# Optimization experiments

Hardware: AMD Instinct MI355X
Metric: run time of the kernel (lower is better)

## Reference

```python
import jax, jax.numpy as jnp
import numpy as np

DIM = 320; D_STATE = 32; D_CONV = 4; HEADDIM = 80; D_INNER = 640; NHEADS = 8
CONV_DIM = D_INNER + 2 * D_STATE          # 704
D_IN_PROJ = 2 * D_INNER + 2 * D_STATE + NHEADS  # 1352
ATTN_HEADS = 4; MLP_DIM = 1024; DEPTH = 2; INNER = DIM // 2  # cross-attn downsample_rate=2
PATCH = (128.0, 256.0, 256.0); IMG = (16, 32, 32); NPTS = 6; BATCH = 2
EPS = 1e-5
TWO_PI = 2.0 * np.pi


def layernorm(x, w, b):
    m = x.mean(-1, keepdims=True)
    v = ((x - m) ** 2).mean(-1, keepdims=True)
    return (x - m) * jax.lax.rsqrt(v + EPS) * w + b


def pe_encode(coords, gauss):
    # coords in [0,1], last dim 3 -> random fourier features (sin|cos) of width DIM
    c = TWO_PI * ((2.0 * coords - 1.0) @ gauss)
    return jnp.concatenate([jnp.sin(c), jnp.cos(c)], -1)


def mha(qi, ki, vi, wq, bq, wk, bk, wv, bv, wo, bo):
    q = qi @ wq.T + bq
    k = ki @ wk.T + bk
    v = vi @ wv.T + bv
    B, Nq, Ci = q.shape
    hd = Ci // ATTN_HEADS
    q = q.reshape(B, Nq, ATTN_HEADS, hd)
    k = k.reshape(B, -1, ATTN_HEADS, hd)
    v = v.reshape(B, -1, ATTN_HEADS, hd)
    att = jax.nn.softmax(jnp.einsum('bqhd,bkhd->bhqk', q, k) / np.sqrt(hd), -1)
    o = jnp.einsum('bhqk,bkhd->bqhd', att, v).reshape(B, Nq, Ci)
    return o @ wo.T + bo


def mamba2(xn, in_w, conv_w, conv_b, dt_bias, A_log, Dp, rms_w, out_w):
    Bt, L, _ = xn.shape
    zxbcdt = xn @ in_w.T                                    # (B,L,1352)
    z, xBC, dt = jnp.split(zxbcdt, [D_INNER, D_INNER + CONV_DIM], axis=-1)
    dt = jax.nn.softplus(dt + dt_bias)                      # (B,L,H)
    # causal depthwise conv over sequence, kernel D_CONV
    pad = jnp.pad(xBC, ((0, 0), (D_CONV - 1, 0), (0, 0)))
    conv = conv_b + sum(pad[:, k:k + L] * conv_w[:, k] for k in range(D_CONV))
    xBC = jax.nn.silu(conv)
    xs, Bm, Cm = jnp.split(xBC, [D_INNER, D_INNER + D_STATE], axis=-1)
    A = -jnp.exp(A_log)                                     # (H,)
    xh = xs.reshape(Bt, L, NHEADS, HEADDIM)

    def step(S, inp):  # S: (B,H,N,P)
        dt_t, x_t, B_t, C_t = inp  # (B,H),(B,H,P),(B,N),(B,N)
        decay = jnp.exp(dt_t * A)
        S = S * decay[..., None, None] + (dt_t[..., None, None] * B_t[:, None, :, None]) * x_t[:, :, None, :]
        y = jnp.einsum('bn,bhnp->bhp', C_t, S)
        return S, y

    S0 = jnp.zeros((Bt, NHEADS, D_STATE, HEADDIM), xn.dtype)
    _, ys = jax.lax.scan(step, S0, (dt.transpose(1, 0, 2), xh.transpose(1, 0, 2, 3), Bm.transpose(1, 0, 2), Cm.transpose(1, 0, 2)))
    y = ys.transpose(1, 0, 2, 3) + Dp[None, None, :, None] * xh  # (B,L,H,P)
    y = y.reshape(Bt, L, D_INNER)
    y = y * jax.nn.silu(z)                                  # gated RMSNorm (norm_before_gate=False)
    y = y * jax.lax.rsqrt((y * y).mean(-1, keepdims=True) + EPS) * rms_w
    return y @ out_w.T


def _forward(x, coords, ln_w, ln_b, in_w, conv_w, conv_b, dt_bias, A_log, Dp, rms_w, out_w,
             pe_gauss, point_tab, sa_w, sa_b, t2i_w, t2i_b, t2i_ow, t2i_ob,
             i2t_w, i2t_b, i2t_ow, i2t_ob, norms_w, norms_b, mlp_w1, mlp_b1, mlp_w2, mlp_b2, labels):
    B, C = x.shape[:2]
    img = x.shape[2:]
    n = int(np.prod(img))
    xf = jnp.transpose(x.reshape(B, C, n), (0, 2, 1))       # (B,n,C)
    keys = mamba2(layernorm(xf, ln_w, ln_b), in_w, conv_w, conv_b, dt_bias, A_log, Dp, rms_w, out_w)
    # point embeddings: fourier PE of normalized click coords + label embedding
    point_emb = pe_encode(coords / jnp.asarray(PATCH, x.dtype), pe_gauss) + point_tab[labels]
    # dense image positional encoding over the feature grid
    axes = [(jnp.arange(s, dtype=x.dtype) + 0.5) / s for s in img]
    grid = jnp.stack(jnp.meshgrid(*axes, indexing='ij'), -1)  # (d,h,w,3)
    kpe = jnp.broadcast_to(pe_encode(grid, pe_gauss).reshape(1, n, C), (B, n, C))
    queries = point_emb
    qpe = point_emb
    for i in range(DEPTH):
        saw, sab = sa_w[i], sa_b[i]
        if i == 0:  # skip_first_layer_pe
            queries = mha(queries, queries, queries, saw[0], sab[0], saw[1], sab[1], saw[2], sab[2], saw[3], sab[3])
        else:
            q = queries + qpe
            queries = queries + mha(q, q, queries, saw[0], sab[0], saw[1], sab[1], saw[2], sab[2], saw[3], sab[3])
        queries = layernorm(queries, norms_w[i, 0], norms_b[i, 0])
        q = queries + qpe
        k = keys + kpe
        queries = queries + mha(q, k, keys, t2i_w[i, 0], t2i_b[i, 0], t2i_w[i, 1], t2i_b[i, 1], t2i_w[i, 2], t2i_b[i, 2], t2i_ow[i], t2i_ob[i])
        queries = layernorm(queries, norms_w[i, 1], norms_b[i, 1])
        queries = queries + jax.nn.relu(queries @ mlp_w1[i].T + mlp_b1[i]) @ mlp_w2[i].T + mlp_b2[i]
        queries = layernorm(queries, norms_w[i, 2], norms_b[i, 2])
        q = queries + qpe
        k = keys + kpe
        keys = keys + mha(k, q, queries, i2t_w[i, 0], i2t_b[i, 0], i2t_w[i, 1], i2t_b[i, 1], i2t_w[i, 2], i2t_b[i, 2], i2t_ow[i], i2t_ob[i])
        keys = layernorm(keys, norms_w[i, 3], norms_b[i, 3])
    return jnp.transpose(keys, (0, 2, 1)).reshape(B, C, *img)


def setup_inputs():
    key = jax.random.key(0)
    ks = iter(jax.random.split(key, 64))
    f32 = jnp.float32

    def nrm(shape, s=0.02):
        return s * jax.random.normal(next(ks), shape, dtype=f32)

    inp = {}
    inp['x'] = jax.random.normal(next(ks), (BATCH, DIM) + IMG, dtype=f32)
    inp['coords'] = jax.random.uniform(next(ks), (BATCH, NPTS, 3), dtype=f32) * jnp.asarray(PATCH, f32)
    inp['labels'] = jax.random.randint(next(ks), (BATCH, NPTS), 0, 2)
    inp['ln_w'] = jnp.ones((DIM,), f32)
    inp['ln_b'] = jnp.zeros((DIM,), f32)
    inp['in_w'] = nrm((D_IN_PROJ, DIM))
    inp['conv_w'] = nrm((CONV_DIM, D_CONV), 0.2)
    inp['conv_b'] = jnp.zeros((CONV_DIM,), f32)
    inp['dt_bias'] = nrm((NHEADS,), 0.1)
    inp['A_log'] = jnp.log(jnp.arange(1, NHEADS + 1, dtype=f32))
    inp['Dp'] = jnp.ones((NHEADS,), f32)
    inp['rms_w'] = jnp.ones((D_INNER,), f32)
    inp['out_w'] = nrm((DIM, D_INNER))
    inp['pe_gauss'] = jax.random.normal(next(ks), (3, DIM // 2), dtype=f32)
    inp['point_tab'] = nrm((2, DIM), 1.0)
    inp['sa_w'] = nrm((DEPTH, 4, DIM, DIM))
    inp['sa_b'] = jnp.zeros((DEPTH, 4, DIM), f32)
    inp['t2i_w'] = nrm((DEPTH, 3, INNER, DIM))
    inp['t2i_b'] = jnp.zeros((DEPTH, 3, INNER), f32)
    inp['t2i_ow'] = nrm((DEPTH, DIM, INNER))
    inp['t2i_ob'] = jnp.zeros((DEPTH, DIM), f32)
    inp['i2t_w'] = nrm((DEPTH, 3, INNER, DIM))
    inp['i2t_b'] = jnp.zeros((DEPTH, 3, INNER), f32)
    inp['i2t_ow'] = nrm((DEPTH, DIM, INNER))
    inp['i2t_ob'] = jnp.zeros((DEPTH, DIM), f32)
    inp['norms_w'] = jnp.ones((DEPTH, 4, DIM), f32)
    inp['norms_b'] = jnp.zeros((DEPTH, 4, DIM), f32)
    inp['mlp_w1'] = nrm((DEPTH, MLP_DIM, DIM))
    inp['mlp_b1'] = jnp.zeros((DEPTH, MLP_DIM), f32)
    inp['mlp_w2'] = nrm((DEPTH, DIM, MLP_DIM))
    inp['mlp_b2'] = jnp.zeros((DEPTH, DIM), f32)
    return inp


def reference(x, coords, labels, ln_w, ln_b, in_w, conv_w, conv_b, dt_bias, A_log, Dp, rms_w, out_w,
              pe_gauss, point_tab, sa_w, sa_b, t2i_w, t2i_b, t2i_ow, t2i_ob,
              i2t_w, i2t_b, i2t_ow, i2t_ob, norms_w, norms_b, mlp_w1, mlp_b1, mlp_w2, mlp_b2):
    return _forward(x, coords, ln_w, ln_b, in_w, conv_w, conv_b, dt_bias, A_log, Dp, rms_w, out_w,
                    pe_gauss, point_tab, sa_w, sa_b, t2i_w, t2i_b, t2i_ow, t2i_ob,
                    i2t_w, i2t_b, i2t_ow, i2t_ob, norms_w, norms_b, mlp_w1, mlp_b1, mlp_w2, mlp_b2, labels)
```

## Files before the change

### kernel.cpp

```cpp
#include <hip/hip_runtime.h>
#include <math.h>

#define LSEQ 16384
#define CDIM 320
#define DIN 640
#define NHH 8
#define CONVD 704
#define XBCW 712
#define YSTR 704
#define QCH 64
#define NCHUNK 256

typedef __bf16 bf16_t;
typedef __bf16 bf16x8 __attribute__((ext_vector_type(8)));
typedef float f32x4 __attribute__((ext_vector_type(4)));

__device__ __forceinline__ float wave_sum(float v) {
#pragma unroll
  for (int o = 32; o > 0; o >>= 1) v += __shfl_down(v, o, 64);
  return v;
}
__device__ __forceinline__ float wave_max(float v) {
#pragma unroll
  for (int o = 32; o > 0; o >>= 1) v = fmaxf(v, __shfl_down(v, o, 64));
  return v;
}
__device__ __forceinline__ float block_sum256(float v, float* red) {
  int tid = threadIdx.x;
  v = wave_sum(v);
  __syncthreads();
  if ((tid & 63) == 0) red[tid >> 6] = v;
  __syncthreads();
  return red[0] + red[1] + red[2] + red[3];
}

__global__ void ws_probe(float* out, float v) { out[0] = v; }

__global__ __launch_bounds__(256) void tln(const float* __restrict__ x,
                                           const float* __restrict__ w,
                                           const float* __restrict__ b,
                                           float* __restrict__ out) {
  __shared__ float sT[32][321];
  int t0 = blockIdx.x * 32;
  int tid = threadIdx.x;
  for (int i = tid; i < 2560; i += 256) {
    int c = i >> 3, j4 = i & 7;
    float4 v = *(const float4*)(x + (size_t)c * LSEQ + t0 + j4 * 4);
    sT[j4 * 4 + 0][c] = v.x;
    sT[j4 * 4 + 1][c] = v.y;
    sT[j4 * 4 + 2][c] = v.z;
    sT[j4 * 4 + 3][c] = v.w;
  }
  __syncthreads();
  int wave = tid >> 6, lane = tid & 63;
  for (int tt = wave; tt < 32; tt += 4) {
    float xv[5];
    float s = 0.f;
#pragma unroll
    for (int k = 0; k < 5; ++k) { xv[k] = sT[tt][lane + 64 * k]; s += xv[k]; }
    s = wave_sum(s); s = __shfl(s, 0, 64);
    float mean = s * (1.f / 320.f);
    float v = 0.f;
#pragma unroll
    for (int k = 0; k < 5; ++k) { float d = xv[k] - mean; v += d * d; }
    v = wave_sum(v); v = __shfl(v, 0, 64);
    float rstd = rsqrtf(v * (1.f / 320.f) + 1e-5f);
    float* op = out + (size_t)(t0 + tt) * CDIM;
#pragma unroll
    for (int k = 0; k < 5; ++k) {
      int i = lane + 64 * k;
      op[i] = (xv[k] - mean) * rstd * w[i] + b[i];
    }
  }
}

__global__ __launch_bounds__(256) void lnt(const float* __restrict__ in,
                                           const float* __restrict__ w,
                                           const float* __restrict__ b,
                                           float* __restrict__ out) {
  __shared__ float sT[CDIM][33];
  int t0 = blockIdx.x * 32;
  int tid = threadIdx.x;
  int wave = tid >> 6, lane = tid & 63;
  for (int tt = wave; tt < 32; tt += 4) {
    const float* xp = in + (size_t)(t0 + tt) * CDIM;
    float x[5];
    float s = 0.f;
#pragma unroll
    for (int k = 0; k < 5; ++k) { x[k] = xp[lane + 64 * k]; s += x[k]; }
    s = wave_sum(s); s = __shfl(s, 0, 64);
    float mean = s * (1.f / 320.f);
    float v = 0.f;
#pragma unroll
    for (int k = 0; k < 5; ++k) { float d = x[k] - mean; v += d * d; }
    v = wave_sum(v); v = __shfl(v, 0, 64);
    float rstd = rsqrtf(v * (1.f / 320.f) + 1e-5f);
#pragma unroll
    for (int k = 0; k < 5; ++k) {
      int i = lane + 64 * k;
      sT[i][tt] = (x[k] - mean) * rstd * w[i] + b[i];
    }
  }
  __syncthreads();
  for (int i = tid; i < 320 * 32; i += 256) {
    int cc = i >> 5, t = i & 31;
    out[(size_t)cc * LSEQ + t0 + t] = sT[cc][t];
  }
}

__global__ __launch_bounds__(256) void ln_rows256(float* __restrict__ io,
                                                  const float* __restrict__ w,
                                                  const float* __restrict__ b,
                                                  int nrows) {
  int row = blockIdx.x * 4 + (threadIdx.x >> 6);
  if (row >= nrows) return;
  float* xp = io + (size_t)row * CDIM;
  int lane = threadIdx.x & 63;
  float x[5];
  float s = 0.f;
#pragma unroll
  for (int k = 0; k < 5; ++k) { x[k] = xp[lane + 64 * k]; s += x[k]; }
  s = wave_sum(s); s = __shfl(s, 0, 64);
  float mean = s * (1.f / 320.f);
  float v = 0.f;
#pragma unroll
  for (int k = 0; k < 5; ++k) { float t = x[k] - mean; v += t * t; }
  v = wave_sum(v); v = __shfl(v, 0, 64);
  float rstd = rsqrtf(v * (1.f / 320.f) + 1e-5f);
#pragma unroll
  for (int k = 0; k < 5; ++k) {
    int i = lane + 64 * k;
    xp[i] = (x[k] - mean) * rstd * w[i] + b[i];
  }
}

__global__ __launch_bounds__(256) void gemm_bf(
    const float* __restrict__ A, const float* __restrict__ W,
    const float* __restrict__ bias, const float* __restrict__ pe,
    float* __restrict__ C, float* __restrict__ C2,
    const float* __restrict__ W2, const float* __restrict__ bias2, int wsplit,
    int M, int N, int K, int lda, int ldc, int nsplit, int ldc2,
    int addC, long long sA, long long sC) {
  int z = blockIdx.z;
  A += (size_t)z * sA;
  C += (size_t)z * sC;
  if (C2) C2 += (size_t)z * sC;
  int gx = gridDim.x;
  int nwg = gx * gridDim.y;
  int lin = blockIdx.y * gx + blockIdx.x;
  int xcd = lin & 7, idx = lin >> 3;
  int q = nwg >> 3, r = nwg & 7;
  int base = (xcd < r) ? xcd * (q + 1) : r * (q + 1) + (xcd - r) * q;
  int lin2 = base + idx;
  int mblk = lin2 / gx, nblk = lin2 % gx;
  int m0 = mblk << 7, n0 = nblk << 6;

  __shared__ __align__(16) bf16_t As[2][4096];
  __shared__ __align__(16) bf16_t Ws[2][2048];
  int tid = threadIdx.x;
  int wave = tid >> 6, lane = tid & 63;
  int fm = lane & 15, quad = lane >> 4;
  int rA = tid >> 1, hA = tid & 1;
  int rW = tid >> 2, qW = tid & 3;
  const float* ag = A + (size_t)(m0 + rA) * lda + hA * 16;
  const float* peg = pe ? pe + (size_t)(m0 + rA) * lda + hA * 16 : (const float*)0;
  int wRow = n0 + rW;
  const float* wg;
  if (wRow < wsplit) wg = W + (size_t)wRow * K + qW * 8;
  else               wg = W2 + (size_t)(wRow - wsplit) * K + qW * 8;
  bool wok = wRow < N;
  int aoff = (rA >> 4) * 512 + (hA * 32 + (rA & 15)) * 8;
  int woff = (rW >> 4) * 512 + (qW * 16 + (rW & 15)) * 8;

  f32x4 acc[2][4];
#pragma unroll
  for (int i = 0; i < 2; ++i)
#pragma unroll
    for (int j = 0; j < 4; ++j) acc[i][j] = (f32x4){0.f, 0.f, 0.f, 0.f};

  float4 pa0, pa1, pa2, pa3, pw0, pw1;
  auto loadG = [&](int k0) {
    pa0 = *(const float4*)(ag + k0);
    pa1 = *(const float4*)(ag + k0 + 4);
    pa2 = *(const float4*)(ag + k0 + 8);
    pa3 = *(const float4*)(ag + k0 + 12);
    if (peg) {
      float4 q0 = *(const float4*)(peg + k0);
      float4 q1 = *(const float4*)(peg + k0 + 4);
      float4 q2 = *(const float4*)(peg + k0 + 8);
      float4 q3 = *(const float4*)(peg + k0 + 12);
      pa0.x += q0.x; pa0.y += q0.y; pa0.z += q0.z; pa0.w += q0.w;
      pa1.x += q1.x; pa1.y += q1.y; pa1.z += q1.z; pa1.w += q1.w;
      pa2.x += q2.x; pa2.y += q2.y; pa2.z += q2.z; pa2.w += q2.w;
      pa3.x += q3.x; pa3.y += q3.y; pa3.z += q3.z; pa3.w += q3.w;
    }
    pw0 = make_float4(0.f, 0.f, 0.f, 0.f);
    pw1 = pw0;
    if (wok) {
      pw0 = *(const float4*)(wg + k0);
      pw1 = *(const float4*)(wg + k0 + 4);
    }
  };
  auto packLDS = [&](int buf) {
    bf16x8 v;
    v[0] = (bf16_t)pa0.x; v[1] = (bf16_t)pa0.y; v[2] = (bf16_t)pa0.z; v[3] = (bf16_t)pa0.w;
    v[4] = (bf16_t)pa1.x; v[5] = (bf16_t)pa1.y; v[6] = (bf16_t)pa1.z; v[7] = (bf16_t)pa1.w;
    *(bf16x8*)&As[buf][aoff] = v;
    v[0] = (bf16_t)pa2.x; v[1] = (bf16_t)pa2.y; v[2] = (bf16_t)pa2.z; v[3] = (bf16_t)pa2.w;
    v[4] = (bf16_t)pa3.x; v[5] = (bf16_t)pa3.y; v[6] = (bf16_t)pa3.z; v[7] = (bf16_t)pa3.w;
    *(bf16x8*)&As[buf][aoff + 128] = v;
    v[0] = (bf16_t)pw0.x; v[1] = (bf16_t)pw0.y; v[2] = (bf16_t)pw0.z; v[3] = (bf16_t)pw0.w;
    v[4] = (bf16_t)pw1.x; v[5] = (bf16_t)pw1.y; v[6] = (bf16_t)pw1.z; v[7] = (bf16_t)pw1.w;
    *(bf16x8*)&Ws[buf][woff] = v;
  };

  int nk = K >> 5;
  loadG(0);
  packLDS(0);
  __syncthreads();
  for (int i = 0; i < nk; ++i) {
    int buf = i & 1;
    bool more = (i + 1 < nk);
    if (more) loadG((i + 1) << 5);
    int ab = wave * 1024 + lane * 8;
    bf16x8 af0 = *(bf16x8*)&As[buf][ab];
    bf16x8 af1 = *(bf16x8*)&As[buf][ab + 512];
    bf16x8 b0 = *(bf16x8*)&Ws[buf][lane * 8];
    bf16x8 b1 = *(bf16x8*)&Ws[buf][512 + lane * 8];
    bf16x8 b2 = *(bf16x8*)&Ws[buf][1024 + lane * 8];
    bf16x8 b3 = *(bf16x8*)&Ws[buf][1536 + lane * 8];
    acc[0][0] = __builtin_amdgcn_mfma_f32_16x16x32_bf16(af0, b0, acc[0][0], 0, 0, 0);
    acc[0][1] = __builtin_amdgcn_mfma_f32_16x16x32_bf16(af0, b1, acc[0][1], 0, 0, 0);
    acc[0][2] = __builtin_amdgcn_mfma_f32_16x16x32_bf16(af0, b2, acc[0][2], 0, 0, 0);
    acc[0][3] = __builtin_amdgcn_mfma_f32_16x16x32_bf16(af0, b3, acc[0][3], 0, 0, 0);
    acc[1][0] = __builtin_amdgcn_mfma_f32_16x16x32_bf16(af1, b0, acc[1][0], 0, 0, 0);
    acc[1][1] = __builtin_amdgcn_mfma_f32_16x16x32_bf16(af1, b1, acc[1][1], 0, 0, 0);
    acc[1][2] = __builtin_amdgcn_mfma_f32_16x16x32_bf16(af1, b2, acc[1][2], 0, 0, 0);
    acc[1][3] = __builtin_amdgcn_mfma_f32_16x16x32_bf16(af1, b3, acc[1][3], 0, 0, 0);
    if (more) {
      packLDS(buf ^ 1);
      __syncthreads();
    }
  }
#pragma unroll
  for (int ms = 0; ms < 2; ++ms)
#pragma unroll
    for (int ns = 0; ns < 4; ++ns) {
      int n = n0 + ns * 16 + fm;
      if (n >= N) continue;
      float bv = 0.f;
      if (n < wsplit) { if (bias) bv = bias[n]; }
      else            { if (bias2) bv = bias2[n - wsplit]; }
      float* Cb;
      int ldcb, nc;
      if (n < nsplit) { Cb = C; ldcb = ldc; nc = n; }
      else           { Cb = C2; ldcb = ldc2; nc = n - nsplit; }
#pragma unroll
      for (int rr = 0; rr < 4; ++rr) {
        int m = m0 + wave * 32 + ms * 16 + quad * 4 + rr;
        float v = acc[ms][ns][rr] + bv;
        size_t off = (size_t)m * ldcb + nc;
        if (addC) v += Cb[off];
        Cb[off] = v;
      }
    }
}

__global__ __launch_bounds__(256) void smallmm(
    const float* __restrict__ A, const float* __restrict__ A2,
    const float* __restrict__ W, const float* __restrict__ bias,
    float* __restrict__ C, int N, int K, int addC, int relu, int a2lim) {
  int wave = threadIdx.x >> 6, lane = threadIdx.x & 63;
  int n = blockIdx.x * 4 + wave;
  if (n >= N) return;
  const float* w = W + (size_t)n * K;
  bool useA2 = (A2 != nullptr) && (n < a2lim);
  float part[12];
#pragma unroll
  for (int m = 0; m < 12; ++m) part[m] = 0.f;
  for (int k0 = 0; k0 < K; k0 += 64) {
    int k = k0 + lane;
    if (k < K) {
      float wv = w[k];
      const float* ap = A + k;
      if (useA2) {
        const float* ap2 = A2 + k;
#pragma unroll
        for (int m = 0; m < 12; ++m)
          part[m] = fmaf(ap[(size_t)m * K] + ap2[(size_t)m * K], wv, part[m]);
      } else {
#pragma unroll
        for (int m = 0; m < 12; ++m)
          part[m] = fmaf(ap[(size_t)m * K], wv, part[m]);
      }
    }
  }
// ... 149 lines not shown
    float cav = cabuf[(size_t)h * LSEQ + t0 + tid];
    sca[tid] = cav;
    sexp[tid] = expf(cav);
  }
  for (int i = tid; i < 2048; i += 256) {
    int j = i >> 5, n = i & 31;
    size_t base = (size_t)(t0 + j) * CONVD;
    sB[j * 40 + n] = (bf16_t)Cv[base + 640 + n];
    sC[j * 40 + n] = (bf16_t)Cv[base + 672 + n];
  }
  for (int i = tid; i < 5120; i += 256) {
    int j = i / 80, p = i % 80;
    sXt[p * 72 + j] = (bf16_t)Cv[(size_t)(t0 + j) * CONVD + h * 80 + p];
  }
  {
    const float* sp = Sprev + (size_t)(h * NCHUNK + c) * 2560;
    for (int i = tid; i < 2560; i += 256) {
      int n = i / 80, p = i % 80;
      sSt[p * 40 + n] = (bf16_t)sp[i];
    }
  }
  __syncthreads();
  int m0 = wave * 16;
  int jbase = m0 + quad * 4;
  bf16x8 afC = *(bf16x8*)&sC[(m0 + fm) * 40 + quad * 8];
  f32x4 accS[4];
#pragma unroll
  for (int nt = 0; nt < 4; ++nt) {
    bf16x8 bf = *(bf16x8*)&sB[(nt * 16 + fm) * 40 + quad * 8];
    f32x4 zero = (f32x4){0.f, 0.f, 0.f, 0.f};
    accS[nt] = __builtin_amdgcn_mfma_f32_16x16x32_bf16(afC, bf, zero, 0, 0, 0);
  }
  float scaj[4];
#pragma unroll
  for (int r = 0; r < 4; ++r) scaj[r] = sca[jbase + r];
#pragma unroll
  for (int nt = 0; nt < 4; ++nt) {
    int s = nt * 16 + fm;
    float dts = sdt[s], scas = sca[s];
#pragma unroll
    for (int r = 0; r < 4; ++r) {
      int j = jbase + r;
      float v = 0.f;
      if (s <= j) v = accS[nt][r] * dts * expf(scaj[r] - scas);
      sP[j * 72 + s] = (bf16_t)v;
    }
  }
  f32x4 acc[5];
#pragma unroll
  for (int pt = 0; pt < 5; ++pt) {
    bf16x8 bf = *(bf16x8*)&sSt[(pt * 16 + fm) * 40 + quad * 8];
    f32x4 zero = (f32x4){0.f, 0.f, 0.f, 0.f};
    acc[pt] = __builtin_amdgcn_mfma_f32_16x16x32_bf16(afC, bf, zero, 0, 0, 0);
  }
  float gj[4];
#pragma unroll
  for (int r = 0; r < 4; ++r) gj[r] = sexp[jbase + r];
#pragma unroll
  for (int pt = 0; pt < 5; ++pt)
#pragma unroll
    for (int r = 0; r < 4; ++r) acc[pt][r] *= gj[r];
  bf16x8 afP0 = *(bf16x8*)&sP[(m0 + fm) * 72 + 0 + quad * 8];
  bf16x8 afP1 = *(bf16x8*)&sP[(m0 + fm) * 72 + 32 + quad * 8];
#pragma unroll
  for (int pt = 0; pt < 5; ++pt) {
    bf16x8 bx0 = *(bf16x8*)&sXt[(pt * 16 + fm) * 72 + 0 + quad * 8];
    bf16x8 bx1 = *(bf16x8*)&sXt[(pt * 16 + fm) * 72 + 32 + quad * 8];
    acc[pt] = __builtin_amdgcn_mfma_f32_16x16x32_bf16(afP0, bx0, acc[pt], 0, 0, 0);
    acc[pt] = __builtin_amdgcn_mfma_f32_16x16x32_bf16(afP1, bx1, acc[pt], 0, 0, 0);
  }
  float dval = Dp[h];
#pragma unroll
  for (int pt = 0; pt < 5; ++pt) {
    int p = pt * 16 + fm;
#pragma unroll
    for (int r = 0; r < 4; ++r) {
      int j = jbase + r;
      float xv = (float)sXt[p * 72 + j];
      Y[(size_t)(t0 + j) * YSTR + h * 80 + p] = acc[pt][r] + dval * xv;
    }
  }
}

__global__ __launch_bounds__(256) void gate_rms(float* __restrict__ Y,
                                                const float* __restrict__ Z,
                                                const float* __restrict__ rms_w) {
  __shared__ float red[4];
  size_t row = blockIdx.x;
  float* y = Y + row * YSTR;
  const float* z = Z + row * DIN;
  float ss = 0.f;
  for (int i = threadIdx.x; i < DIN; i += 256) {
    float zi = z[i];
    float g = y[i] * (zi / (1.f + expf(-zi)));
    y[i] = g;
    ss += g * g;
  }
  float tot = block_sum256(ss, red);
  float r = rsqrtf(tot / (float)DIN + 1e-5f);
  for (int i = threadIdx.x; i < DIN; i += 256) y[i] = y[i] * r * rms_w[i];
}

__global__ void kpe_kernel(const float* __restrict__ gauss, float* __restrict__ KPE) {
  int idx = blockIdx.x * 256 + threadIdx.x;
  if (idx >= LSEQ * 160) return;
  int f = idx % 160, t = idx / 160;
  int d = t >> 10, hh = (t >> 5) & 31, w = t & 31;
  float vx = 2.f * ((d + 0.5f) / 16.f) - 1.f;
  float vy = 2.f * ((hh + 0.5f) / 32.f) - 1.f;
  float vz = 2.f * ((w + 0.5f) / 32.f) - 1.f;
  float cc = 6.28318530717958647692f * (vx * gauss[f] + vy * gauss[160 + f] + vz * gauss[320 + f]);
  KPE[(size_t)t * CDIM + f] = sinf(cc);
  KPE[(size_t)t * CDIM + 160 + f] = cosf(cc);
}

__global__ void point_kernel(const float* __restrict__ coords, const int* __restrict__ labels,
                             const float* __restrict__ gauss, const float* __restrict__ ptab,
                             float* __restrict__ qpe, float* __restrict__ queries) {
  int idx = blockIdx.x * 64 + threadIdx.x;
  if (idx >= 12 * 160) return;
  int f = idx % 160, pt = idx / 160;
  const float* co = coords + pt * 3;
  float vx = 2.f * (co[0] / 128.f) - 1.f;
  float vy = 2.f * (co[1] / 256.f) - 1.f;
  float vz = 2.f * (co[2] / 256.f) - 1.f;
  float cc = 6.28318530717958647692f * (vx * gauss[f] + vy * gauss[160 + f] + vz * gauss[320 + f]);
  int lab = labels[pt];
  float sv = sinf(cc) + ptab[lab * CDIM + f];
  float cv = cosf(cc) + ptab[lab * CDIM + 160 + f];
  qpe[pt * CDIM + f] = sv;       qpe[pt * CDIM + 160 + f] = cv;
  queries[pt * CDIM + f] = sv;   queries[pt * CDIM + 160 + f] = cv;
}

__global__ void attn_self(const float* __restrict__ P3, float* __restrict__ O) {
  int h = blockIdx.x, b = blockIdx.y;
  __shared__ float sq[6][80], sk[6][80], sv[6][80], sw[6][6];
  int tid = threadIdx.x;
  for (int i = tid; i < 480; i += 128) {
    int tok = i / 80, p = i % 80;
    const float* base = P3 + (size_t)(b * 6 + tok) * 960 + h * 80 + p;
    sq[tok][p] = base[0]; sk[tok][p] = base[320]; sv[tok][p] = base[640];
  }
  __syncthreads();
  if (tid < 36) {
    int qi = tid / 6, ki = tid % 6;
    float d = 0.f;
    for (int p = 0; p < 80; ++p) d += sq[qi][p] * sk[ki][p];
    sw[qi][ki] = d * 0.11180339887498948f;
  }
  __syncthreads();
  if (tid < 6) {
    float mx = sw[tid][0];
    for (int k = 1; k < 6; ++k) mx = fmaxf(mx, sw[tid][k]);
    float s = 0.f;
    for (int k = 0; k < 6; ++k) { float e = expf(sw[tid][k] - mx); sw[tid][k] = e; s += e; }
    float inv = 1.f / s;
    for (int k = 0; k < 6; ++k) sw[tid][k] *= inv;
  }
  __syncthreads();
  for (int i = tid; i < 480; i += 128) {
    int qi = i / 80, p = i % 80;
    float o = 0.f;
    for (int k = 0; k < 6; ++k) o += sw[qi][k] * sv[k][p];
    O[(size_t)(b * 6 + qi) * CDIM + h * 80 + p] = o;
  }
}

__global__ __launch_bounds__(256) void attn_t2i_part2(const float* __restrict__ Qp,
                                                      const float* __restrict__ Kp,
                                                      const float* __restrict__ Vp,
                                                      float* __restrict__ Part) {
  int b = blockIdx.z, h = blockIdx.y, c = blockIdx.x;
  Qp += (size_t)b * 960;
  Kp += (size_t)b * LSEQ * 160;
  Vp += (size_t)b * LSEQ * 160;
  Part += (size_t)b * 24 * 64 * 42;
  __shared__ float sq[240];
  __shared__ float redm[4][6], reds[4][6];
  __shared__ __align__(16) bf16_t sPb[16 * 264];
  __shared__ __align__(16) bf16_t sVtb[48 * 264];
  int tid = threadIdx.x;
  int wave = tid >> 6, lane = tid & 63;
  if (tid < 240) sq[tid] = Qp[(size_t)(tid / 40) * 160 + h * 40 + (tid % 40)];
// ... 29 lines not shown
    if (lane == 0) redm[wave][qi] = wm;
  }
  __syncthreads();
  float gmax[6], ls[6];
#pragma unroll
  for (int qi = 0; qi < 6; ++qi)
    gmax[qi] = fmaxf(fmaxf(redm[0][qi], redm[1][qi]), fmaxf(redm[2][qi], redm[3][qi]));
#pragma unroll
  for (int qi = 0; qi < 6; ++qi) {
    float e = expf(s[qi] - gmax[qi]);
    sPb[qi * 264 + tid] = (bf16_t)e;
    float wsum = wave_sum(e);
    if (lane == 0) reds[wave][qi] = wsum;
  }
  __syncthreads();
#pragma unroll
  for (int qi = 0; qi < 6; ++qi)
    ls[qi] = reds[0][qi] + reds[1][qi] + reds[2][qi] + reds[3][qi];
  if (tid == 0) {
#pragma unroll
    for (int qi = 0; qi < 6; ++qi) {
      float* pml = Part + (size_t)((h * 6 + qi) * 64 + c) * 42;
      pml[40] = gmax[qi];
      pml[41] = ls[qi];
    }
  }
  if (wave == 0) {
    int fm = lane & 15, quad = lane >> 4;
    f32x4 acc[3];
#pragma unroll
    for (int nt = 0; nt < 3; ++nt) acc[nt] = (f32x4){0.f, 0.f, 0.f, 0.f};
#pragma unroll
    for (int ks = 0; ks < 8; ++ks) {
      bf16x8 a = *(bf16x8*)&sPb[fm * 264 + ks * 32 + quad * 8];
#pragma unroll
      for (int nt = 0; nt < 3; ++nt) {
        bf16x8 bb = *(bf16x8*)&sVtb[(nt * 16 + fm) * 264 + ks * 32 + quad * 8];
        acc[nt] = __builtin_amdgcn_mfma_f32_16x16x32_bf16(a, bb, acc[nt], 0, 0, 0);
      }
    }
#pragma unroll
    for (int nt = 0; nt < 3; ++nt)
#pragma unroll
      for (int r = 0; r < 4; ++r) {
        int qi = quad * 4 + r;
        int p = nt * 16 + fm;
        if (qi < 6 && p < 40)
          Part[(size_t)((h * 6 + qi) * 64 + c) * 42 + p] = acc[nt][r];
      }
  }
}

__global__ void attn_t2i_comb(const float* __restrict__ Part, float* __restrict__ O) {
  int b = blockIdx.y;
  int blk = blockIdx.x;
  int qi = blk % 6;
  int h = blk / 6;
  int j = threadIdx.x;
  const float* base = Part + (size_t)b * 24 * 64 * 42 + (size_t)blk * 64 * 42;
  float m = base[j * 42 + 40], l = base[j * 42 + 41];
  float gmax = wave_max(m);
  gmax = __shfl(gmax, 0, 64);
  float sc = expf(m - gmax);
  float tot = wave_sum(l * sc);
  tot = __shfl(tot, 0, 64);
  float inv = 1.f / tot;
  __shared__ float ssc[64];
  ssc[j] = sc;
  __syncthreads();
  if (j < 40) {
    float a0 = 0.f, a1 = 0.f, a2 = 0.f, a3 = 0.f;
    for (int jj = 0; jj < 64; jj += 4) {
      a0 = fmaf(base[(jj + 0) * 42 + j], ssc[jj + 0], a0);
      a1 = fmaf(base[(jj + 1) * 42 + j], ssc[jj + 1], a1);
      a2 = fmaf(base[(jj + 2) * 42 + j], ssc[jj + 2], a2);
      a3 = fmaf(base[(jj + 3) * 42 + j], ssc[jj + 3], a3);
    }
    O[(size_t)b * 960 + (size_t)qi * 160 + h * 40 + j] = (a0 + a1 + a2 + a3) * inv;
  }
}

__global__ __launch_bounds__(256) void attn_i2t(const float* __restrict__ Qp,
                                                const float* __restrict__ KV,
                                                float* __restrict__ O) {
  int h = blockIdx.y, b = blockIdx.z;
  int t = blockIdx.x * 256 + threadIdx.x;
  Qp += (size_t)b * LSEQ * 160;
  O += (size_t)b * LSEQ * 160;
  __shared__ float sk[6][40], sv[6][40];
  if (threadIdx.x < 240) {
    int tok = threadIdx.x / 40, p = threadIdx.x % 40;
    const float* base = KV + (size_t)(b * 6 + tok) * 320 + h * 40 + p;
    sk[tok][p] = base[0];
    sv[tok][p] = base[160];
  }
  __syncthreads();
  const float* q = Qp + (size_t)t * 160 + h * 40;
  float qr[40];
#pragma unroll
  for (int v = 0; v < 10; ++v) {
    float4 q4 = *(const float4*)(q + v * 4);
    qr[v * 4 + 0] = q4.x; qr[v * 4 + 1] = q4.y; qr[v * 4 + 2] = q4.z; qr[v * 4 + 3] = q4.w;
  }
  float s[6];
#pragma unroll
  for (int k = 0; k < 6; ++k) {
    float d = 0.f;
    for (int p = 0; p < 40; ++p) d += qr[p] * sk[k][p];
    s[k] = d * 0.15811388300841897f;
  }
  float mx = s[0];
#pragma unroll
  for (int k = 1; k < 6; ++k) mx = fmaxf(mx, s[k]);
  float sum = 0.f;
#pragma unroll
  for (int k = 0; k < 6; ++k) { s[k] = expf(s[k] - mx); sum += s[k]; }
  float inv = 1.f / sum;
  float* o = O + (size_t)t * 160 + h * 40;
#pragma unroll
  for (int v = 0; v < 10; ++v) {
    float o0 = 0.f, o1 = 0.f, o2 = 0.f, o3 = 0.f;
#pragma unroll
    for (int k = 0; k < 6; ++k) {
      float w = s[k];
      o0 += w * sv[k][v * 4 + 0];
      o1 += w * sv[k][v * 4 + 1];
      o2 += w * sv[k][v * 4 + 2];
      o3 += w * sv[k][v * 4 + 3];
    }
    *(float4*)(o + v * 4) = make_float4(o0 * inv, o1 * inv, o2 * inv, o3 * inv);
  }
}

extern "C" void kernel_launch(void* const* d_in, const int* in_sizes, int n_in,
                              void* d_out, int out_size, void* d_ws, size_t ws_size,
                              hipStream_t stream) {
  (void)in_sizes; (void)n_in; (void)out_size;
  const float* x       = (const float*)d_in[0];
  const float* coords  = (const float*)d_in[1];
  const int*   labels  = (const int*)  d_in[2];
  const float* ln_w    = (const float*)d_in[3];
  const float* ln_b    = (const float*)d_in[4];
  const float* in_w    = (const float*)d_in[5];
  const float* conv_w  = (const float*)d_in[6];
  const float* conv_b  = (const float*)d_in[7];
  const float* dt_bias = (const float*)d_in[8];
  const float* A_log   = (const float*)d_in[9];
  const float* Dp      = (const float*)d_in[10];
  const float* rms_w   = (const float*)d_in[11];
  const float* out_w   = (const float*)d_in[12];
  const float* gauss   = (const float*)d_in[13];
  const float* ptab    = (const float*)d_in[14];
  const float* sa_w    = (const float*)d_in[15];
  const float* sa_b    = (const float*)d_in[16];
  const float* t2i_w   = (const float*)d_in[17];
  const float* t2i_b   = (const float*)d_in[18];
  const float* t2i_ow  = (const float*)d_in[19];
  const float* t2i_ob  = (const float*)d_in[20];
  const float* i2t_w   = (const float*)d_in[21];
  const float* i2t_b   = (const float*)d_in[22];
  const float* i2t_ow  = (const float*)d_in[23];
  const float* i2t_ob  = (const float*)d_in[24];
  const float* norms_w = (const float*)d_in[25];
  const float* norms_b = (const float*)d_in[26];
  const float* mlp_w1  = (const float*)d_in[27];
  const float* mlp_b1  = (const float*)d_in[28];
  const float* mlp_w2  = (const float*)d_in[29];
  const float* mlp_b2  = (const float*)d_in[30];
  float* out = (float*)d_out;
  float* ws = (float*)d_ws;

  const size_t NEED = (size_t)(10485760 + 5242880 + 11665408 + 11534336 + 10485760 +
                               131072 + 131072 + 65536) * 4;
  if (ws_size < NEED) {
    ws_probe<<<1, 1, 0, stream>>>(out, (float)ws_size);
    return;
  }
  float* R_K = ws;
  float* P   = ws + 10485760;
  float* XN_     = P;
  float* SCHUNK_ = P;
  float* ZB_     = P + 5242880;
  float* XBC_    = P + 15728640;
  float* SPREV_  = P + 15728640;
  float* CV_     = P + 27394048;
  float* DT_     = P + 38928384;
  float* CA_     = P + 39059456;
  float* KPE_  = P;
  float* T0_   = P + 5242880;
  float* T3_   = P + 10485760;
  float* T1_   = P + 15728640;
  float* T2_   = P + 26214400;
  float* PART_ = P + 36700160;
  float* SM_   = P + 36829184;
  float* QPE_  = SM_;
  float* QRY_  = SM_ + 3840;
  float* P3_   = SM_ + 7680;
  float* PO_   = SM_ + 19200;
  float* H_    = SM_ + 23040;
  float* Q160_ = SM_ + 35328;
  float* O160_ = SM_ + 37248;
  float* KV_   = SM_ + 39168;

  const long long sIMG160 = (long long)LSEQ * 160;
  const long long sIMG320 = (long long)LSEQ * CDIM;
  const int NOSPLIT = 1 << 30;

  for (int b = 0; b < 2; ++b) {
    const float* xb = x + (size_t)b * CDIM * LSEQ;
    float* Kb = R_K + (size_t)b * LSEQ * CDIM;

    tln<<<LSEQ / 32, 256, 0, stream>>>(xb, ln_w, ln_b, XN_);

    gemm_bf<<<dim3(22, 128, 1), 256, 0, stream>>>(
        XN_, in_w, nullptr, nullptr, ZB_, XBC_, nullptr, nullptr, NOSPLIT,
        LSEQ, 1352, CDIM, CDIM, DIN, DIN, XBCW, 0, 0, 0);

    dt_kernel<<<LSEQ * NHH / 256, 256, 0, stream>>>(XBC_, dt_bias, DT_);
    conv2<<<dim3(11, 128), 256, 0, stream>>>(XBC_, conv_w, conv_b, CV_);

    scan_a<<<dim3(NCHUNK, NHH), 256, 0, stream>>>(CV_, DT_, A_log, SCHUNK_, CA_);
    scan_b<<<dim3(10, NHH), 256, 0, stream>>>(SCHUNK_, CA_, SPREV_);
    scan_c<<<dim3(NCHUNK, NHH), 256, 0, stream>>>(CV_, DT_, CA_, SPREV_, Dp, CV_);

    gate_rms<<<LSEQ, 256, 0, stream>>>(CV_, ZB_, rms_w);

    gemm_bf<<<dim3(5, 128, 1), 256, 0, stream>>>(
        CV_, out_w, nullptr, nullptr, Kb, nullptr, nullptr, nullptr, NOSPLIT,
        LSEQ, CDIM, DIN, YSTR, CDIM, NOSPLIT, 0, 0, 0, 0);
  }

  kpe_kernel<<<LSEQ * 160 / 256, 256, 0, stream>>>(gauss, KPE_);
  point_kernel<<<30, 64, 0, stream>>>(coords, labels, gauss, ptab, QPE_, QRY_);

  for (int i = 0; i < 2; ++i) {
    const float* saw = sa_w + (size_t)i * 4 * CDIM * CDIM;
    const float* sab = sa_b + (size_t)i * 4 * CDIM;
    smallmm<<<240, 256, 0, stream>>>(QRY_, (i == 0) ? nullptr : QPE_,
                                     saw, sab, P3_, 960, CDIM, 0, 0, 640);
    attn_self<<<dim3(4, 2), 128, 0, stream>>>(P3_, PO_);
    smallmm<<<80, 256, 0, stream>>>(PO_, nullptr, saw + 3 * 102400, sab + 3 * CDIM,
                                    QRY_, CDIM, CDIM, (i == 0) ? 0 : 1, 0, 0);
    ln_rows256<<<3, 256, 0, stream>>>(QRY_, norms_w + (size_t)(i * 4 + 0) * CDIM,
                                      norms_b + (size_t)(i * 4 + 0) * CDIM, 12);

    smallmm<<<40, 256, 0, stream>>>(QRY_, QPE_, t2i_w + (size_t)(i * 3 + 0) * 51200,
                                    t2i_b + (size_t)(i * 3 + 0) * 160, Q160_,
                                    160, CDIM, 0, 0, 160);
    gemm_bf<<<dim3(5, 128, 2), 256, 0, stream>>>(
        R_K, t2i_w + (size_t)(i * 3 + 1) * 51200, t2i_b + (size_t)(i * 3 + 1) * 160,
        KPE_, T0_, T3_, i2t_w + (size_t)(i * 3 + 0) * 51200,
        i2t_b + (size_t)(i * 3 + 0) * 160, 160,
        LSEQ, 320, CDIM, CDIM, 160, 160, 160, 0, sIMG320, sIMG160);
    gemm_bf<<<dim3(3, 128, 2), 256, 0, stream>>>(
        R_K, t2i_w + (size_t)(i * 3 + 2) * 51200, t2i_b + (size_t)(i * 3 + 2) * 160,
        nullptr, T1_, nullptr, nullptr, nullptr, NOSPLIT,
        LSEQ, 160, CDIM, CDIM, 160, NOSPLIT, 0, 0, sIMG320, sIMG160);
    attn_t2i_part2<<<dim3(64, 4, 2), 256, 0, stream>>>(Q160_, T0_, T1_, PART_);
    attn_t2i_comb<<<dim3(24, 2), 64, 0, stream>>>(PART_, O160_);
    smallmm<<<80, 256, 0, stream>>>(O160_, nullptr, t2i_ow + (size_t)i * 51200,
                                    t2i_ob + (size_t)i * CDIM, QRY_,
                                    CDIM, 160, 1, 0, 0);
    ln_rows256<<<3, 256, 0, stream>>>(QRY_, norms_w + (size_t)(i * 4 + 1) * CDIM,
                                      norms_b + (size_t)(i * 4 + 1) * CDIM, 12);

    smallmm<<<256, 256, 0, stream>>>(QRY_, nullptr, mlp_w1 + (size_t)i * 1024 * CDIM,
                                     mlp_b1 + (size_t)i * 1024, H_, 1024, CDIM, 0, 1, 0);
    smallmm<<<80, 256, 0, stream>>>(H_, nullptr, mlp_w2 + (size_t)i * CDIM * 1024,
                                    mlp_b2 + (size_t)i * CDIM, QRY_, CDIM, 1024, 1, 0, 0);
    ln_rows256<<<3, 256, 0, stream>>>(QRY_, norms_w + (size_t)(i * 4 + 2) * CDIM,
                                      norms_b + (size_t)(i * 4 + 2) * CDIM, 12);

    smallmm<<<80, 256, 0, stream>>>(QRY_, QPE_, i2t_w + (size_t)(i * 3 + 1) * 51200,
                                    i2t_b + (size_t)(i * 3 + 1) * 160, KV_,
                                    320, CDIM, 0, 0, 160);
    attn_i2t<<<dim3(LSEQ / 256, 4, 2), 256, 0, stream>>>(T3_, KV_, T2_);
    gemm_bf<<<dim3(5, 128, 2), 256, 0, stream>>>(
        T2_, i2t_ow + (size_t)i * CDIM * 160, i2t_ob + (size_t)i * CDIM,
        nullptr, R_K, nullptr, nullptr, nullptr, NOSPLIT,
        LSEQ, CDIM, 160, 160, CDIM, NOSPLIT, 0, 1, sIMG160, sIMG320);
    if (i == 0) {
      ln_rows256<<<2 * LSEQ / 4, 256, 0, stream>>>(
          R_K, norms_w + (size_t)3 * CDIM, norms_b + (size_t)3 * CDIM, 2 * LSEQ);
    }
  }

  for (int b = 0; b < 2; ++b) {
    lnt<<<LSEQ / 32, 256, 0, stream>>>(
        R_K + (size_t)b * LSEQ * CDIM, norms_w + (size_t)7 * CDIM,
        norms_b + (size_t)7 * CDIM, out + (size_t)b * CDIM * LSEQ);
  }
}
```

Measured before the change: 1.037 ms.

## Store GEMM activation inputs and weights in bf16 to halve load traffic

Producers of GEMM inputs (tln, gate_rms, attn_i2t) now write bf16 instead of fp32, and the in/out projection weights are converted to bf16 by a small cvt_bf kernel before use. gemm_bf gains abf/wbf flags so it can load bf16 directly and skip the per-element conversion during LDS packing. The goal is to cut global memory traffic and conversion work in the memory-bound GEMMs. The cost is extra weight-conversion launches on every call, plus bf16 rounding of the intermediates, which the old code already applied inside the GEMM anyway.

```diff
diff --git a/kernel.cpp b/kernel.cpp
--- a/kernel.cpp
+++ b/kernel.cpp
@@ -13,6 +13,7 @@
 
 typedef __bf16 bf16_t;
 typedef __bf16 bf16x8 __attribute__((ext_vector_type(8)));
+typedef __bf16 bf16x4 __attribute__((ext_vector_type(4)));
 typedef float f32x4 __attribute__((ext_vector_type(4)));
 
 __device__ __forceinline__ float wave_sum(float v) {
@@ -36,10 +37,19 @@
 
 __global__ void ws_probe(float* out, float v) { out[0] = v; }
 
+__global__ void cvt_bf(const float* __restrict__ src, bf16_t* __restrict__ dst, int n) {
+  int i = (blockIdx.x * 256 + threadIdx.x) * 4;
+  if (i >= n) return;
+  float4 v = *(const float4*)(src + i);
+  bf16x4 o;
+  o[0] = (bf16_t)v.x; o[1] = (bf16_t)v.y; o[2] = (bf16_t)v.z; o[3] = (bf16_t)v.w;
+  *(bf16x4*)(dst + i) = o;
+}
+
 __global__ __launch_bounds__(256) void tln(const float* __restrict__ x,
                                            const float* __restrict__ w,
                                            const float* __restrict__ b,
-                                           float* __restrict__ out) {
+                                           bf16_t* __restrict__ out) {
   __shared__ float sT[32][321];
   int t0 = blockIdx.x * 32;
   int tid = threadIdx.x;
@@ -65,11 +75,11 @@
     for (int k = 0; k < 5; ++k) { float d = xv[k] - mean; v += d * d; }
     v = wave_sum(v); v = __shfl(v, 0, 64);
     float rstd = rsqrtf(v * (1.f / 320.f) + 1e-5f);
-    float* op = out + (size_t)(t0 + tt) * CDIM;
+    bf16_t* op = out + (size_t)(t0 + tt) * CDIM;
 #pragma unroll
     for (int k = 0; k < 5; ++k) {
       int i = lane + 64 * k;
-      op[i] = (xv[k] - mean) * rstd * w[i] + b[i];
+      op[i] = (bf16_t)((xv[k] - mean) * rstd * w[i] + b[i]);
     }
   }
 }
@@ -135,14 +145,13 @@
 }
 
 __global__ __launch_bounds__(256) void gemm_bf(
-    const float* __restrict__ A, const float* __restrict__ W,
+    const void* __restrict__ A, const void* __restrict__ W,
     const float* __restrict__ bias, const float* __restrict__ pe,
     float* __restrict__ C, float* __restrict__ C2,
-    const float* __restrict__ W2, const float* __restrict__ bias2, int wsplit,
+    const void* __restrict__ W2, const float* __restrict__ bias2, int wsplit,
     int M, int N, int K, int lda, int ldc, int nsplit, int ldc2,
-    int addC, long long sA, long long sC) {
+    int addC, int abf, int wbf, long long sA, long long sC) {
   int z = blockIdx.z;
-  A += (size_t)z * sA;
   C += (size_t)z * sC;
   if (C2) C2 += (size_t)z * sC;
   int gx = gridDim.x;
@@ -162,13 +171,25 @@
   int fm = lane & 15, quad = lane >> 4;
   int rA = tid >> 1, hA = tid & 1;
   int rW = tid >> 2, qW = tid & 3;
-  const float* ag = A + (size_t)(m0 + rA) * lda + hA * 16;
-  const float* peg = pe ? pe + (size_t)(m0 + rA) * lda + hA * 16 : (const float*)0;
+  const float* ag = nullptr;
+  const bf16_t* agb = nullptr;
+  const float* peg = nullptr;
+  if (abf) {
+    agb = (const bf16_t*)A + (size_t)z * sA + (size_t)(m0 + rA) * lda + hA * 16;
+  } else {
+    ag = (const float*)A + (size_t)z * sA + (size_t)(m0 + rA) * lda + hA * 16;
+    if (pe) peg = pe + (size_t)(m0 + rA) * lda + hA * 16;
+  }
   int wRow = n0 + rW;
-  const float* wg;
-  if (wRow < wsplit) wg = W + (size_t)wRow * K + qW * 8;
-  else               wg = W2 + (size_t)(wRow - wsplit) * K + qW * 8;
   bool wok = wRow < N;
+  const float* wg = nullptr;
+  const bf16_t* wgb = nullptr;
+  {
+    const void* Wsel = (wRow < wsplit) ? W : W2;
+    int wr = (wRow < wsplit) ? wRow : wRow - wsplit;
+    if (wbf) wgb = (const bf16_t*)Wsel + (size_t)wr * K + qW * 8;
+    else     wg  = (const float*)Wsel + (size_t)wr * K + qW * 8;
+  }
   int aoff = (rA >> 4) * 512 + (hA * 32 + (rA & 15)) * 8;
   int woff = (rW >> 4) * 512 + (qW * 16 + (rW & 15)) * 8;
 
@@ -178,40 +199,57 @@
 #pragma unroll
     for (int j = 0; j < 4; ++j) acc[i][j] = (f32x4){0.f, 0.f, 0.f, 0.f};
 
+  bf16x8 ra0, ra1, rw;
   float4 pa0, pa1, pa2, pa3, pw0, pw1;
   auto loadG = [&](int k0) {
-    pa0 = *(const float4*)(ag + k0);
-    pa1 = *(const float4*)(ag + k0 + 4);
-    pa2 = *(const float4*)(ag + k0 + 8);
-    pa3 = *(const float4*)(ag + k0 + 12);
-    if (peg) {
-      float4 q0 = *(const float4*)(peg + k0);
-      float4 q1 = *(const float4*)(peg + k0 + 4);
-      float4 q2 = *(const float4*)(peg + k0 + 8);
-      float4 q3 = *(const float4*)(peg + k0 + 12);
-      pa0.x += q0.x; pa0.y += q0.y; pa0.z += q0.z; pa0.w += q0.w;
-      pa1.x += q1.x; pa1.y += q1.y; pa1.z += q1.z; pa1.w += q1.w;
-      pa2.x += q2.x; pa2.y += q2.y; pa2.z += q2.z; pa2.w += q2.w;
-      pa3.x += q3.x; pa3.y += q3.y; pa3.z += q3.z; pa3.w += q3.w;
-    }
-    pw0 = make_float4(0.f, 0.f, 0.f, 0.f);
-    pw1 = pw0;
-    if (wok) {
-      pw0 = *(const float4*)(wg + k0);
-      pw1 = *(const float4*)(wg + k0 + 4);
+    if (abf) {
+      ra0 = *(const bf16x8*)(agb + k0);
+      ra1 = *(const bf16x8*)(agb + k0 + 8);
+    } else {
+      pa0 = *(const float4*)(ag + k0);
+      pa1 = *(const float4*)(ag + k0 + 4);
+      pa2 = *(const float4*)(ag + k0 + 8);
+      pa3 = *(const float4*)(ag + k0 + 12);
+      if (peg) {
+        float4 q0 = *(const float4*)(peg + k0);
+        float4 q1 = *(const float4*)(peg + k0 + 4);
+        float4 q2 = *(const float4*)(peg + k0 + 8);
+        float4 q3 = *(const float4*)(peg + k0 + 12);
+        pa0.x += q0.x; pa0.y += q0.y; pa0.z += q0.z; pa0.w += q0.w;
+        pa1.x += q1.x; pa1.y += q1.y; pa1.z += q1.z; pa1.w += q1.w;
+        pa2.x += q2.x; pa2.y += q2.y; pa2.z += q2.z; pa2.w += q2.w;
+        pa3.x += q3.x; pa3.y += q3.y; pa3.z += q3.z; pa3.w += q3.w;
+      }
+    }
+    if (wbf) {
+      if (wok) rw = *(const bf16x8*)(wgb + k0);
+      else {
+#pragma unroll
+        for (int j = 0; j < 8; ++j) rw[j] = (bf16_t)0.f;
+      }
+    } else {
+      pw0 = make_float4(0.f, 0.f, 0.f, 0.f);
+      pw1 = pw0;
+      if (wok) {
+        pw0 = *(const float4*)(wg + k0);
+        pw1 = *(const float4*)(wg + k0 + 4);
+      }
     }
   };
   auto packLDS = [&](int buf) {
-    bf16x8 v;
-    v[0] = (bf16_t)pa0.x; v[1] = (bf16_t)pa0.y; v[2] = (bf16_t)pa0.z; v[3] = (bf16_t)pa0.w;
-    v[4] = (bf16_t)pa1.x; v[5] = (bf16_t)pa1.y; v[6] = (bf16_t)pa1.z; v[7] = (bf16_t)pa1.w;
-    *(bf16x8*)&As[buf][aoff] = v;
-    v[0] = (bf16_t)pa2.x; v[1] = (bf16_t)pa2.y; v[2] = (bf16_t)pa2.z; v[3] = (bf16_t)pa2.w;
-    v[4] = (bf16_t)pa3.x; v[5] = (bf16_t)pa3.y; v[6] = (bf16_t)pa3.z; v[7] = (bf16_t)pa3.w;
-    *(bf16x8*)&As[buf][aoff + 128] = v;
-    v[0] = (bf16_t)pw0.x; v[1] = (bf16_t)pw0.y; v[2] = (bf16_t)pw0.z; v[3] = (bf16_t)pw0.w;
-    v[4] = (bf16_t)pw1.x; v[5] = (bf16_t)pw1.y; v[6] = (bf16_t)pw1.z; v[7] = (bf16_t)pw1.w;
-    *(bf16x8*)&Ws[buf][woff] = v;
+    if (!abf) {
+      ra0[0] = (bf16_t)pa0.x; ra0[1] = (bf16_t)pa0.y; ra0[2] = (bf16_t)pa0.z; ra0[3] = (bf16_t)pa0.w;
+      ra0[4] = (bf16_t)pa1.x; ra0[5] = (bf16_t)pa1.y; ra0[6] = (bf16_t)pa1.z; ra0[7] = (bf16_t)pa1.w;
+      ra1[0] = (bf16_t)pa2.x; ra1[1] = (bf16_t)pa2.y; ra1[2] = (bf16_t)pa2.z; ra1[3] = (bf16_t)pa2.w;
+      ra1[4] = (bf16_t)pa3.x; ra1[5] = (bf16_t)pa3.y; ra1[6] = (bf16_t)pa3.z; ra1[7] = (bf16_t)pa3.w;
+    }
+    *(bf16x8*)&As[buf][aoff] = ra0;
+    *(bf16x8*)&As[buf][aoff + 128] = ra1;
+    if (!wbf) {
+      rw[0] = (bf16_t)pw0.x; rw[1] = (bf16_t)pw0.y; rw[2] = (bf16_t)pw0.z; rw[3] = (bf16_t)pw0.w;
+      rw[4] = (bf16_t)pw1.x; rw[5] = (bf16_t)pw1.y; rw[6] = (bf16_t)pw1.z; rw[7] = (bf16_t)pw1.w;
+    }
+    *(bf16x8*)&Ws[buf][woff] = rw;
   };
 
   int nk = K >> 5;
@@ -527,23 +565,33 @@
   }
 }
 
-__global__ __launch_bounds__(256) void gate_rms(float* __restrict__ Y,
+__global__ __launch_bounds__(256) void gate_rms(const float* __restrict__ Y,
                                                 const float* __restrict__ Z,
-                                                const float* __restrict__ rms_w) {
+                                                const float* __restrict__ rms_w,
+                                                bf16_t* __restrict__ YB) {
   __shared__ float red[4];
   size_t row = blockIdx.x;
-  float* y = Y + row * YSTR;
+  const float* y = Y + row * YSTR;
   const float* z = Z + row * DIN;
-  float ss = 0.f;
-  for (int i = threadIdx.x; i < DIN; i += 256) {
-    float zi = z[i];
-    float g = y[i] * (zi / (1.f + expf(-zi)));
-    y[i] = g;
-    ss += g * g;
-  }
+  bf16_t* yo = YB + row * DIN;
+  int tid = threadIdx.x;
+  float g0, g1, g2 = 0.f;
+  {
+    float zi = z[tid];
+    g0 = y[tid] * (zi / (1.f + expf(-zi)));
+    zi = z[tid + 256];
+    g1 = y[tid + 256] * (zi / (1.f + expf(-zi)));
+    if (tid + 512 < DIN) {
+      zi = z[tid + 512];
+      g2 = y[tid + 512] * (zi / (1.f + expf(-zi)));
+    }
+  }
+  float ss = g0 * g0 + g1 * g1 + g2 * g2;
   float tot = block_sum256(ss, red);
   float r = rsqrtf(tot / (float)DIN + 1e-5f);
-  for (int i = threadIdx.x; i < DIN; i += 256) y[i] = y[i] * r * rms_w[i];
+  yo[tid] = (bf16_t)(g0 * r * rms_w[tid]);
+  yo[tid + 256] = (bf16_t)(g1 * r * rms_w[tid + 256]);
+  if (tid + 512 < DIN) yo[tid + 512] = (bf16_t)(g2 * r * rms_w[tid + 512]);
 }
 
 __global__ void kpe_kernel(const float* __restrict__ gauss, float* __restrict__ KPE) {
@@ -739,7 +787,7 @@
 
 __global__ __launch_bounds__(256) void attn_i2t(const float* __restrict__ Qp,
                                                 const float* __restrict__ KV,
-                                                float* __restrict__ O) {
+                                                bf16_t* __restrict__ O) {
   int h = blockIdx.y, b = blockIdx.z;
   int t = blockIdx.x * 256 + threadIdx.x;
   Qp += (size_t)b * LSEQ * 160;
@@ -773,7 +821,7 @@
 #pragma unroll
   for (int k = 0; k < 6; ++k) { s[k] = expf(s[k] - mx); sum += s[k]; }
   float inv = 1.f / sum;
-  float* o = O + (size_t)t * 160 + h * 40;
+  bf16_t* o = O + (size_t)t * 160 + h * 40;
 #pragma unroll
   for (int v = 0; v < 10; ++v) {
     float o0 = 0.f, o1 = 0.f, o2 = 0.f, o3 = 0.f;
@@ -785,7 +833,10 @@
       o2 += w * sv[k][v * 4 + 2];
       o3 += w * sv[k][v * 4 + 3];
     }
-    *(float4*)(o + v * 4) = make_float4(o0 * inv, o1 * inv, o2 * inv, o3 * inv);
+    bf16x4 ov;
+    ov[0] = (bf16_t)(o0 * inv); ov[1] = (bf16_t)(o1 * inv);
+    ov[2] = (bf16_t)(o2 * inv); ov[3] = (bf16_t)(o3 * inv);
+    *(bf16x4*)(o + v * 4) = ov;
   }
 }
 
@@ -835,21 +886,23 @@
   }
   float* R_K = ws;
   float* P   = ws + 10485760;
-  float* XN_     = P;
+  bf16_t* XNB_   = (bf16_t*)P;
   float* SCHUNK_ = P;
   float* ZB_     = P + 5242880;
   float* XBC_    = P + 15728640;
   float* SPREV_  = P + 15728640;
+  bf16_t* YB_    = (bf16_t*)(P + 20971520);
   float* CV_     = P + 27394048;
   float* DT_     = P + 38928384;
   float* CA_     = P + 39059456;
-  float* KPE_  = P;
-  float* T0_   = P + 5242880;
-  float* T3_   = P + 10485760;
-  float* T1_   = P + 15728640;
-  float* T2_   = P + 26214400;
-  float* PART_ = P + 36700160;
-  float* SM_   = P + 36829184;
+  bf16_t* WBM_   = (bf16_t*)(P + 38928384);
+  float* KPE_   = P;
+  float* T0_    = P + 5242880;
+  float* T3_    = P + 10485760;
+  float* T1_    = P + 15728640;
+  bf16_t* T2B_  = (bf16_t*)(P + 26214400);
+  float* PART_  = P + 36700160;
+  float* SM_    = P + 36829184;
   float* QPE_  = SM_;
   float* QRY_  = SM_ + 3840;
   float* P3_   = SM_ + 7680;
@@ -867,11 +920,12 @@
     const float* xb = x + (size_t)b * CDIM * LSEQ;
     float* Kb = R_K + (size_t)b * LSEQ * CDIM;
 
-    tln<<<LSEQ / 32, 256, 0, stream>>>(xb, ln_w, ln_b, XN_);
+    tln<<<LSEQ / 32, 256, 0, stream>>>(xb, ln_w, ln_b, XNB_);
+    cvt_bf<<<(432640 / 4 + 255) / 256, 256, 0, stream>>>(in_w, WBM_, 432640);
 
     gemm_bf<<<dim3(22, 128, 1), 256, 0, stream>>>(
-        XN_, in_w, nullptr, nullptr, ZB_, XBC_, nullptr, nullptr, NOSPLIT,
-        LSEQ, 1352, CDIM, CDIM, DIN, DIN, XBCW, 0, 0, 0);
+        XNB_, WBM_, nullptr, nullptr, ZB_, XBC_, nullptr, nullptr, NOSPLIT,
+        LSEQ, 1352, CDIM, CDIM, DIN, DIN, XBCW, 0, 1, 1, 0, 0);
 
     dt_kernel<<<LSEQ * NHH / 256, 256, 0, stream>>>(XBC_, dt_bias, DT_);
     conv2<<<dim3(11, 128), 256, 0, stream>>>(XBC_, conv_w, conv_b, CV_);
@@ -880,11 +934,12 @@
     scan_b<<<dim3(10, NHH), 256, 0, stream>>>(SCHUNK_, CA_, SPREV_);
     scan_c<<<dim3(NCHUNK, NHH), 256, 0, stream>>>(CV_, DT_, CA_, SPREV_, Dp, CV_);
 
-    gate_rms<<<LSEQ, 256, 0, stream>>>(CV_, ZB_, rms_w);
+    cvt_bf<<<(204800 / 4 + 255) / 256, 256, 0, stream>>>(out_w, WBM_, 204800);
+    gate_rms<<<LSEQ, 256, 0, stream>>>(CV_, ZB_, rms_w, YB_);
 
     gemm_bf<<<dim3(5, 128, 1), 256, 0, stream>>>(
-        CV_, out_w, nullptr, nullptr, Kb, nullptr, nullptr, nullptr, NOSPLIT,
-        LSEQ, CDIM, DIN, YSTR, CDIM, NOSPLIT, 0, 0, 0, 0);
+        YB_, WBM_, nullptr, nullptr, Kb, nullptr, nullptr, nullptr, NOSPLIT,
+        LSEQ, CDIM, DIN, DIN, CDIM, NOSPLIT, 0, 0, 1, 1, 0, 0);
   }
 
   kpe_kernel<<<LSEQ * 160 / 256, 256, 0, stream>>>(gauss, KPE_);
@@ -908,11 +963,11 @@
         R_K, t2i_w + (size_t)(i * 3 + 1) * 51200, t2i_b + (size_t)(i * 3 + 1) * 160,
         KPE_, T0_, T3_, i2t_w + (size_t)(i * 3 + 0) * 51200,
         i2t_b + (size_t)(i * 3 + 0) * 160, 160,
-        LSEQ, 320, CDIM, CDIM, 160, 160, 160, 0, sIMG320, sIMG160);
+        LSEQ, 320, CDIM, CDIM, 160, 160, 160, 0, 0, 0, sIMG320, sIMG160);
     gemm_bf<<<dim3(3, 128, 2), 256, 0, stream>>>(
         R_K, t2i_w + (size_t)(i * 3 + 2) * 51200, t2i_b + (size_t)(i * 3 + 2) * 160,
         nullptr, T1_, nullptr, nullptr, nullptr, NOSPLIT,
-        LSEQ, 160, CDIM, CDIM, 160, NOSPLIT, 0, 0, sIMG320, sIMG160);
+        LSEQ, 160, CDIM, CDIM, 160, NOSPLIT, 0, 0, 0, 0, sIMG320, sIMG160);
     attn_t2i_part2<<<dim3(64, 4, 2), 256, 0, stream>>>(Q160_, T0_, T1_, PART_);
     attn_t2i_comb<<<dim3(24, 2), 64, 0, stream>>>(PART_, O160_);
     smallmm<<<80, 256, 0, stream>>>(O160_, nullptr, t2i_ow + (size_t)i * 51200,
@@ -931,11 +986,11 @@
     smallmm<<<80, 256, 0, stream>>>(QRY_, QPE_, i2t_w + (size_t)(i * 3 + 1) * 51200,
                                     i2t_b + (size_t)(i * 3 + 1) * 160, KV_,
                                     320, CDIM, 0, 0, 160);
-    attn_i2t<<<dim3(LSEQ / 256, 4, 2), 256, 0, stream>>>(T3_, KV_, T2_);
+    attn_i2t<<<dim3(LSEQ / 256, 4, 2), 256, 0, stream>>>(T3_, KV_, T2B_);
     gemm_bf<<<dim3(5, 128, 2), 256, 0, stream>>>(
-        T2_, i2t_ow + (size_t)i * CDIM * 160, i2t_ob + (size_t)i * CDIM,
+        T2B_, i2t_ow + (size_t)i * CDIM * 160, i2t_ob + (size_t)i * CDIM,
         nullptr, R_K, nullptr, nullptr, nullptr, NOSPLIT,
-        LSEQ, CDIM, 160, 160, CDIM, NOSPLIT, 0, 1, sIMG160, sIMG320);
+        LSEQ, CDIM, 160, 160, CDIM, NOSPLIT, 0, 1, 1, 0, sIMG160, sIMG320);
     if (i == 0) {
       ln_rows256<<<2 * LSEQ / 4, 256, 0, stream>>>(
           R_K, norms_w + (size_t)3 * CDIM, norms_b + (size_t)3 * CDIM, 2 * LSEQ);
```

Result: no change. 1.036 ms (-0.1%).
